# Optimization experiments

Hardware: AMD Instinct MI355X
Metric: run time of the kernel (lower is better)

The kernel has to match this reference:

```python
import jax, jax.numpy as jnp
import numpy as np

N_NODES = 100000
N_EDGES = 1600000
HIDDEN = 64
N_LAYERS = 3
N_CLASSES = 2
N_GRAPHS = 128
NEG_SLOPE = 0.2  # PyG GATConv default negative_slope


def setup_inputs() -> dict:
    key = jax.random.key(0)
    ks = jax.random.split(key, 8)
    x = jax.random.randint(ks[0], (N_NODES,), 0, 2)
    edge_index = jax.random.randint(ks[1], (2, N_EDGES), 0, N_NODES)
    batch = jnp.sort(jax.random.randint(ks[2], (N_NODES,), 0, N_GRAPHS))
    scale = 1.0 / np.sqrt(HIDDEN)
    embed_table = jax.random.normal(ks[3], (2, HIDDEN), jnp.float32)
    Ws = jax.random.normal(ks[4], (N_LAYERS, HIDDEN, HIDDEN), jnp.float32) * scale
    a_srcs = jax.random.normal(ks[5], (N_LAYERS, HIDDEN), jnp.float32) * scale
    a_dsts = jax.random.normal(ks[6], (N_LAYERS, HIDDEN), jnp.float32) * scale
    biases = jnp.zeros((N_LAYERS, HIDDEN), jnp.float32)
    W_out = jax.random.normal(ks[7], (HIDDEN, N_CLASSES), jnp.float32) * scale
    b_out = jnp.zeros((N_CLASSES,), jnp.float32)
    return {"x": x, "edge_index": edge_index, "batch": batch,
            "embed_table": embed_table, "Ws": Ws, "a_srcs": a_srcs,
            "a_dsts": a_dsts, "biases": biases, "W_out": W_out, "b_out": b_out}


def _gat_layer(h, src, dst, W, a_s, a_d, b):
    # h: [N, D]; src/dst: [E'] (self loops included) -> PyG GATConv, heads=1
    hW = h @ W                                   # [N, D]
    e = jax.nn.leaky_relu((hW @ a_s)[src] + (hW @ a_d)[dst], NEG_SLOPE)  # [E']
    m = jax.ops.segment_max(e, dst, num_segments=N_NODES)               # stable softmax per dst
    ex = jnp.exp(e - m[dst])
    denom = jax.ops.segment_sum(ex, dst, num_segments=N_NODES)
    alpha = ex / denom[dst]                      # [E']
    out = jax.ops.segment_sum(hW[src] * alpha[:, None], dst, num_segments=N_NODES)
    return out + b


def reference(x, edge_index, batch, embed_table, Ws, a_srcs, a_dsts, biases, W_out, b_out):
    loop = jnp.arange(N_NODES)
    src = jnp.concatenate([edge_index[0], loop])  # PyG add_self_loops=True
    dst = jnp.concatenate([edge_index[1], loop])
    h = embed_table[x]                            # [N, D]
    for l in range(N_LAYERS):
        h = _gat_layer(h, src, dst, Ws[l], a_srcs[l], a_dsts[l], biases[l])
        if l < N_LAYERS - 1:
            h = jax.nn.relu(h)
    sums = jax.ops.segment_sum(h, batch, num_segments=N_GRAPHS)
    counts = jax.ops.segment_sum(jnp.ones((N_NODES,), h.dtype), batch, num_segments=N_GRAPHS)
    pooled = sums / jnp.maximum(counts, 1.0)[:, None]  # global_mean_pool
    return pooled @ W_out + b_out                      # [G, num_classes]
```

## Files before the change

### kernel.cpp

```cpp
#include <hip/hip_runtime.h>
#include <hip/hip_bf16.h>
#include <float.h>

#define N_NODES 100000
#define N_EDGES 1600000
#define HIDDEN 64
#define N_GRAPHS 128
#define NEG_SLOPE 0.2f
#define ETOT (N_EDGES + N_NODES)

#define BSHIFT 9
#define NB ((N_NODES + 511) >> BSHIFT)
#define PAIR_CHUNK 4096
#define PAIR_BLOCKS ((N_EDGES + PAIR_CHUNK - 1) / PAIR_CHUNK)
#define XBIT_BLOCKS ((N_NODES + 255) / 256)
#define TBL_BLOCKS (NLVL / 8)
#define CAP 12288

#define NREP 64
#define REP_STRIDE 272
#define NLVL 512

__device__ __forceinline__ int sb0(unsigned u) { return (int)((unsigned)(u << 24)) >> 24; }
__device__ __forceinline__ int sb1(unsigned u) { return (int)((unsigned)(u << 16)) >> 24; }
__device__ __forceinline__ int sb2(unsigned u) { return (int)((unsigned)(u << 8)) >> 24; }
__device__ __forceinline__ int sb3(unsigned u) { return (int)u >> 24; }


__global__ __launch_bounds__(256) void k_prep(
    const int* __restrict__ x,
    int* __restrict__ gcnt, float* __restrict__ pool_acc,
    unsigned* __restrict__ xb)
{
    int t = threadIdx.x, b = blockIdx.x;
    if (b == 0 && t < NB) gcnt[t] = 0;
    if (b < NREP && t < 2 * N_GRAPHS) pool_acc[b * REP_STRIDE + t] = 0.f;
    int i = b * 256 + t;
    int lane = t & 63;
    bool bb = (i < N_NODES) && (x[i] != 0);
    unsigned long long m = __ballot(bb);
    int wid = i >> 6;
    if (i < N_NODES + 64) {
        if (lane == 0) xb[wid * 2] = (unsigned)m;
        if (lane == 32) xb[wid * 2 + 1] = (unsigned)(m >> 32);
    }
}


__global__ __launch_bounds__(512) void k_scatter(
    const int* __restrict__ e0, const int* __restrict__ e1,
    const unsigned* __restrict__ xb, int* __restrict__ gcnt,
    int* __restrict__ pairs,
    const float* __restrict__ embed, const float* __restrict__ Ws,
    const float* __restrict__ biases, const float* __restrict__ a_srcs,
    const float* __restrict__ a_dsts, const float* __restrict__ W_out,
    unsigned char* __restrict__ Tq8, float* __restrict__ Tscl,
    float* __restrict__ Ts1s, float* __restrict__ Ts1d,
    float* __restrict__ sparams, float* __restrict__ Vp)
{
    __shared__ int hcnt[NB];
    __shared__ int base[NB];
    __shared__ int lstart[NB];
    __shared__ int tot[256];
    __shared__ int staged[PAIR_CHUNK];
    __shared__ int sdest[PAIR_CHUNK];
    int t = threadIdx.x, b = blockIdx.x;

    if (b >= PAIR_BLOCKS + TBL_BLOCKS) {
        int w = t >> 6, f = t & 63;
        if (w < 4) {
            const float* W3 = Ws + 8192;
            float s = 0.f;
#pragma unroll 8
            for (int m = 0; m < 64; ++m) {
                float u = (w == 0) ? a_srcs[128 + m]
                        : (w == 1) ? W_out[2 * m]
                        : (w == 2) ? W_out[2 * m + 1]
                        : a_dsts[128 + m];
                s = fmaf(W3[f * 64 + m], u, s);
            }
            Vp[f * 4 + w] = s;
        }
        return;
    }

    if (b >= PAIR_BLOCKS) {
        int l = (b - PAIR_BLOCKS) * 8 + (t >> 6);
        int f = t & 63;
        float r0 = 0.f, r1 = 0.f;
#pragma unroll 8
        for (int k = 0; k < 64; ++k) {
            float w = Ws[k * 64 + f];
            r0 = fmaf(embed[k], w, r0);
            r1 = fmaf(embed[64 + k], w, r1);
        }
        if (l == 0) {
            float as = a_srcs[f], ad = a_dsts[f];
            float t0 = r0 * as, t1 = r1 * as, t2 = r0 * ad, t3 = r1 * ad;
#pragma unroll
            for (int off = 32; off >= 1; off >>= 1) {
                t0 += __shfl_xor(t0, off); t1 += __shfl_xor(t1, off);
                t2 += __shfl_xor(t2, off); t3 += __shfl_xor(t3, off);
            }
            if (f == 0) { sparams[0] = t0; sparams[1] = t1; sparams[2] = t2; sparams[3] = t3; }
        }
        if (l == 1) {
            float b2 = biases[128 + f];
            float t4 = b2 * W_out[f * 2];
            float t5 = b2 * W_out[f * 2 + 1];
#pragma unroll
            for (int off = 32; off >= 1; off >>= 1) {
                t4 += __shfl_xor(t4, off); t5 += __shfl_xor(t5, off);
            }
            if (f == 0) { sparams[4] = t4; sparams[5] = t5; }
        }
        float c1 = (float)l * (1.f / (NLVL - 1));
        float o = fmaxf(biases[f] + r0 + c1 * (r1 - r0), 0.f);
        const float* W1 = Ws + 4096;
        float h = 0.f;
#pragma unroll 8
        for (int k = 0; k < 64; ++k) h = fmaf(__shfl(o, k), W1[k * 64 + f], h);
        float ss = h * a_srcs[64 + f];
        float sd = h * a_dsts[64 + f];
        float am = fabsf(h);
#pragma unroll
        for (int off = 32; off >= 1; off >>= 1) {
            ss += __shfl_xor(ss, off);
            sd += __shfl_xor(sd, off);
            am = fmaxf(am, __shfl_xor(am, off));
        }
        float iscl = (am > 0.f) ? 127.f / am : 0.f;
        Tq8[l * 64 + f] = (unsigned char)(__float2int_rn(h * iscl) & 255);
        if (f == 0) { Tscl[l] = am * (1.f / 127.f); Ts1s[l] = ss; Ts1d[l] = sd; }
        return;
    }

    if (t < NB) hcnt[t] = 0;
    __syncthreads();
    int ebase = b * PAIR_CHUNK;
    int ecount = min(PAIR_CHUNK, N_EDGES - ebase);
    for (int i = 4 * t; i < ecount; i += 2048) {
        int4 d4 = *(const int4*)(e1 + ebase + i);
        atomicAdd(&hcnt[d4.x >> BSHIFT], 1);
        atomicAdd(&hcnt[d4.y >> BSHIFT], 1);
        atomicAdd(&hcnt[d4.z >> BSHIFT], 1);
        atomicAdd(&hcnt[d4.w >> BSHIFT], 1);
    }
    __syncthreads();
    int v = (t < NB) ? hcnt[t] : 0;
    if (t < 256) tot[t] = v;
    __syncthreads();
    for (int off = 1; off < 256; off <<= 1) {
        int u = (t >= off && t < 256) ? tot[t - off] : 0;
        __syncthreads();
        if (t < 256) tot[t] += u;
        __syncthreads();
    }
    if (t < NB) {
        lstart[t] = tot[t] - v;
        base[t] = v ? atomicAdd(&gcnt[t], v) : 0;
        hcnt[t] = 0;
    }
    __syncthreads();
    for (int i = 4 * t; i < ecount; i += 2048) {
        int4 s4 = *(const int4*)(e0 + ebase + i);
        int4 d4 = *(const int4*)(e1 + ebase + i);
        int ss[4] = {s4.x, s4.y, s4.z, s4.w};
        int dd[4] = {d4.x, d4.y, d4.z, d4.w};
#pragma unroll
        for (int j = 0; j < 4; ++j) {
            int s = ss[j], d = dd[j];
            int xv = (xb[s >> 5] >> (s & 31)) & 1;
            int B = d >> BSHIFT;
            int idx = atomicAdd(&hcnt[B], 1);
            int lp = lstart[B] + idx;
            staged[lp] = (xv << 26) | ((d & 511) << 17) | s;
            sdest[lp] = B * CAP + base[B] + idx;
        }
    }
    __syncthreads();
    for (int i = t; i < ecount; i += 512)
        pairs[sdest[i]] = staged[i];
}

__global__ __launch_bounds__(1024) void k_csr_bucket(
    const int* __restrict__ pairs, const int* __restrict__ gcnt,
    const int* __restrict__ x, const float* __restrict__ sparams,
    int* __restrict__ rowptr, int* __restrict__ col,
    unsigned short* __restrict__ cidx)
{
    __shared__ int deg[512];
    __shared__ int excl[512];
    __shared__ int cnt2[512];
    __shared__ int wsum[16];
    __shared__ int p0sh;
    int b = blockIdx.x;
    int t = threadIdx.x;
    int nb = b << BSHIFT;
    int nodes = min(512, N_NODES - nb);

    int pv = (t < b) ? gcnt[t] : 0;
#pragma unroll
    for (int off = 32; off >= 1; off >>= 1) pv += __shfl_xor(pv, off);
    if ((t & 63) == 0) wsum[t >> 6] = pv;
    __syncthreads();
    if (t == 0) {
        int s = 0;
#pragma unroll
        for (int i = 0; i < 16; ++i) s += wsum[i];
        p0sh = s;
    }

    int xself = 0;
    if (t < 512) {
        xself = (t < nodes) ? (x[nb + t] & 1) : 0;
        deg[t] = (t < nodes) ? (1 | (xself << 16)) : 0;
        cnt2[t] = 1;
    }
    __syncthreads();
    int cnt = gcnt[b];
    int pbase = b * CAP;
    int cnt4 = cnt & ~3;
    for (int i = 4 * t; i < cnt4; i += 4096) {
        int4 p4 = *(const int4*)(pairs + pbase + i);
        atomicAdd(&deg[(p4.x >> 17) & 511], 1 | (((p4.x >> 26) & 1) << 16));
        atomicAdd(&deg[(p4.y >> 17) & 511], 1 | (((p4.y >> 26) & 1) << 16));
        atomicAdd(&deg[(p4.z >> 17) & 511], 1 | (((p4.z >> 26) & 1) << 16));
        atomicAdd(&deg[(p4.w >> 17) & 511], 1 | (((p4.w >> 26) & 1) << 16));
    }
    for (int i = cnt4 + t; i < cnt; i += 1024) {
        int p = pairs[pbase + i];
        atomicAdd(&deg[(p >> 17) & 511], 1 | (((p >> 26) & 1) << 16));
    }
    __syncthreads();

    int packed = (t < 512) ? deg[t] : 0;
    int val = packed & 0xFFFF;
    int kx = packed >> 16;
    if (t < nodes) {
        float ss0 = sparams[0], ss1 = sparams[1];
        float sd = xself ? sparams[3] : sparams[2];
        float e0 = ss0 + sd; e0 = (e0 >= 0.f) ? e0 : NEG_SLOPE * e0;
        float e1 = ss1 + sd; e1 = (e1 >= 0.f) ? e1 : NEG_SLOPE * e1;
        float pp0 = __expf(e0), pp1 = __expf(e1);
        float kn = (float)kx, dn = (float)(val - kx);
        float c1 = kn * pp1 / (dn * pp0 + kn * pp1);
        cidx[nb + t] = (unsigned short)__float2int_rn(c1 * (float)(NLVL - 1));
    }

    int xx = val;
#pragma unroll
    for (int off = 1; off < 64; off <<= 1) {
        int y = __shfl_up(xx, off);
        if ((t & 63) >= off) xx += y;
    }
    if ((t & 63) == 63 && t < 512) wsum[t >> 6] = xx;
    __syncthreads();
    if (t == 0) {
        int s = 0;
#pragma unroll
        for (int i = 0; i < 8; ++i) { int v = wsum[i]; wsum[i] = s; s += v; }
    }
    __syncthreads();
    int ex = xx - val + wsum[t >> 6];
    if (t < 512) excl[t] = ex;

    int p0 = p0sh;
    int colbase = p0 + nb;
    if (t < nodes) {
        rowptr[nb + t] = colbase + ex;
        col[colbase + ex] = nb + t;
    }
    if (b == NB - 1 && t == 0) rowptr[N_NODES] = ETOT;
    __syncthreads();
    for (int i = 4 * t; i < cnt4; i += 4096) {
        int4 p4 = *(const int4*)(pairs + pbase + i);
        int pp[4] = {p4.x, p4.y, p4.z, p4.w};
#pragma unroll
        for (int j = 0; j < 4; ++j) {
            int li = (pp[j] >> 17) & 511;
            int pos = colbase + excl[li] + atomicAdd(&cnt2[li], 1);
            col[pos] = pp[j] & 0x1FFFF;
        }
    }
    for (int i = cnt4 + t; i < cnt; i += 1024) {
        int p = pairs[pbase + i];
        int li = (p >> 17) & 511;
        int pos = colbase + excl[li] + atomicAdd(&cnt2[li], 1);
        col[pos] = p & 0x1FFFF;
    }
}


__global__ __launch_bounds__(256) void k_agg1(
    const unsigned char* __restrict__ Tq8, const float* __restrict__ Tscl,
    const float* __restrict__ Ts1s, const float* __restrict__ Ts1d,
    const unsigned short* __restrict__ cidx, const int* __restrict__ col,
    const int* __restrict__ rowptr, const float* __restrict__ bias,
    const float4* __restrict__ Vp, float4* __restrict__ szz)
{
    __shared__ float2 stash[4][64];
    int t = threadIdx.x;
    int wave = t >> 6, lane = t & 63;
    int h = lane >> 5, hl = lane & 31;
    int base = blockIdx.x * 8 + wave * 2;
    if (base >= N_NODES) return;
    const char* hb = (const char*)Tq8;

    int node = base + h;
    bool valid = (node < N_NODES);
    int row = 0, end = 0;
    if (valid) { row = rowptr[node]; end = rowptr[node + 1]; }
    int deg = end - row;
    int degO = __shfl_xor(deg, 32);
    bool fast = (deg <= 32) && (degO <= 32);

    if (fast) {
        int idx = 0;
        float p = 0.f, sc = 0.f;
        if (hl < deg) idx = cidx[col[row + hl]];
        float sdi = Ts1d[__shfl(idx, h * 32)];
        if (hl < deg) {
            float ee = Ts1s[idx] + sdi;
            ee = (ee >= 0.f) ? ee : NEG_SLOPE * ee;
            p = __expf(ee);
            sc = Tscl[idx];
        }
        stash[wave][lane] = make_float2(p * sc, __int_as_float(idx * 64));

        int q = hl >> 4;
        int f = hl & 15;
        int f4 = f * 4;
        int sb = h * 32;
        float a0 = 0.f, a1 = 0.f, a2 = 0.f, a3 = 0.f;
        int degr = (deg + 7) & ~7;
        for (int j = q; j < degr; j += 8) {
            float2 e0 = stash[wave][sb + j];
            float2 e1 = stash[wave][sb + j + 2];
            float2 e2 = stash[wave][sb + j + 4];
            float2 e3 = stash[wave][sb + j + 6];
            unsigned v0 = *(const unsigned*)(hb + (__float_as_int(e0.y) + f4));
            unsigned v1 = *(const unsigned*)(hb + (__float_as_int(e1.y) + f4));
            unsigned v2 = *(const unsigned*)(hb + (__float_as_int(e2.y) + f4));
            unsigned v3 = *(const unsigned*)(hb + (__float_as_int(e3.y) + f4));
            a0 = fmaf(e0.x, (float)sb0(v0), a0);
            a1 = fmaf(e0.x, (float)sb1(v0), a1);
            a2 = fmaf(e0.x, (float)sb2(v0), a2);
            a3 = fmaf(e0.x, (float)sb3(v0), a3);
            a0 = fmaf(e1.x, (float)sb0(v1), a0);
            a1 = fmaf(e1.x, (float)sb1(v1), a1);
            a2 = fmaf(e1.x, (float)sb2(v1), a2);
            a3 = fmaf(e1.x, (float)sb3(v1), a3);
            a0 = fmaf(e2.x, (float)sb0(v2), a0);
            a1 = fmaf(e2.x, (float)sb1(v2), a1);
            a2 = fmaf(e2.x, (float)sb2(v2), a2);
            a3 = fmaf(e2.x, (float)sb3(v2), a3);
            a0 = fmaf(e3.x, (float)sb0(v3), a0);
            a1 = fmaf(e3.x, (float)sb1(v3), a1);
            a2 = fmaf(e3.x, (float)sb2(v3), a2);
            a3 = fmaf(e3.x, (float)sb3(v3), a3);
        }
        float denom = p;
#pragma unroll
        for (int off = 16; off >= 1; off >>= 1) denom += __shfl_xor(denom, off);
        float inv = 1.f / denom;
        a0 += __shfl_xor(a0, 16);
        a1 += __shfl_xor(a1, 16);
        a2 += __shfl_xor(a2, 16);
        a3 += __shfl_xor(a3, 16);

        float4 pr = make_float4(0.f, 0.f, 0.f, 0.f);
        if (hl < 16 && valid) {
            float4 bb = *(const float4*)&bias[4 * f];
            float h0 = fmaxf(fmaf(a0, inv, bb.x), 0.f);
            float h1 = fmaxf(fmaf(a1, inv, bb.y), 0.f);
            float h2 = fmaxf(fmaf(a2, inv, bb.z), 0.f);
            float h3 = fmaxf(fmaf(a3, inv, bb.w), 0.f);
            float4 w0 = Vp[4 * f + 0];
            float4 w1 = Vp[4 * f + 1];
            float4 w2 = Vp[4 * f + 2];
            float4 w3 = Vp[4 * f + 3];
            pr.x = h0 * w0.x + h1 * w1.x + h2 * w2.x + h3 * w3.x;
            pr.y = h0 * w0.y + h1 * w1.y + h2 * w2.y + h3 * w3.y;
            pr.z = h0 * w0.z + h1 * w1.z + h2 * w2.z + h3 * w3.z;
            pr.w = h0 * w0.w + h1 * w1.w + h2 * w2.w + h3 * w3.w;
        }
#pragma unroll
        for (int off = 8; off >= 1; off >>= 1) {
            pr.x += __shfl_xor(pr.x, off);
            pr.y += __shfl_xor(pr.y, off);
            pr.z += __shfl_xor(pr.z, off);
            pr.w += __shfl_xor(pr.w, off);
        }
        if (hl == 0 && valid) szz[node] = pr;
    } else {
        for (int s = 0; s < 2; ++s) {
            int nd = base + s;
            if (nd >= N_NODES) continue;
            int r = rowptr[nd], e = rowptr[nd + 1];
            float sdi = Ts1d[cidx[nd]];
            float m = -FLT_MAX;
            for (int j = r + lane; j < e; j += 64) {
                float ee = Ts1s[cidx[col[j]]] + sdi;
                ee = (ee >= 0.f) ? ee : NEG_SLOPE * ee;
                m = fmaxf(m, ee);
            }
#pragma unroll
            for (int off = 32; off >= 1; off >>= 1) m = fmaxf(m, __shfl_xor(m, off));
            float denom = 0.f;
            for (int j = r + lane; j < e; j += 64) {
                float ee = Ts1s[cidx[col[j]]] + sdi;
                ee = (ee >= 0.f) ? ee : NEG_SLOPE * ee;
                denom += __expf(ee - m);
            }
#pragma unroll
            for (int off = 32; off >= 1; off >>= 1) denom += __shfl_xor(denom, off);
            float inv = 1.f / denom;
            float acc = 0.f;
            for (int j = r; j < e; ++j) {
                int idxj = cidx[col[j]];
                float ee = Ts1s[idxj] + sdi;
                ee = (ee >= 0.f) ? ee : NEG_SLOPE * ee;
                float w = __expf(ee - m) * inv * Tscl[idxj];
                int bq = (int)(signed char)Tq8[idxj * 64 + lane];
                acc = fmaf(w, (float)bq, acc);
            }
            float hv = fmaxf(acc + bias[lane], 0.f);
            float4 vp = Vp[lane];
            float4 pr = make_float4(hv * vp.x, hv * vp.y, hv * vp.z, hv * vp.w);
#pragma unroll
            for (int off = 32; off >= 1; off >>= 1) {
                pr.x += __shfl_xor(pr.x, off);
                pr.y += __shfl_xor(pr.y, off);
                pr.z += __shfl_xor(pr.z, off);
                pr.w += __shfl_xor(pr.w, off);
            }
            if (lane == 0) szz[nd] = pr;
        }
    }
}


__global__ __launch_bounds__(256) void k_pool2(
    const float4* __restrict__ szz, const int* __restrict__ col,
    const int* __restrict__ rowptr, const int* __restrict__ batch,
    float* __restrict__ pool_acc)
{
    __shared__ int rp2[33];
    int t = threadIdx.x;
    int wave = t >> 6, lane = t & 63;
    int h = lane >> 5, hl = lane & 31;
    int nb0 = blockIdx.x * 32;
    if (t < 33) {
        int n = nb0 + t;
        rp2[t] = (n <= N_NODES) ? rowptr[n] : ETOT;
    }
    __syncthreads();
    float* rep = pool_acc + ((blockIdx.x * 4 + wave) & (NREP - 1)) * REP_STRIDE;

    int gcur = -1;
    float acc0 = 0.f, acc1 = 0.f;

#pragma unroll
    for (int i = 0; i < 4; ++i) {
        int nls = wave * 8 + 2 * i + h;
        int node = nb0 + nls;
        bool valid = (node < N_NODES);
        int row = valid ? rp2[nls] : 0;
        int end = valid ? rp2[nls + 1] : 0;
        int deg = end - row;
        int degO = __shfl_xor(deg, 32);
        bool fast = (deg <= 32) && (degO <= 32);
        float r0 = 0.f, r1 = 0.f;

        if (fast) {
            float sdi = valid ? szz[node].w : 0.f;
            float p = 0.f, zy = 0.f, zz = 0.f;
            if (hl < deg) {
                int c = col[row + hl];
                float4 sz = szz[c];
                float ee = sz.x + sdi;
                ee = (ee >= 0.f) ? ee : NEG_SLOPE * ee;
                p = __expf(ee);
                zy = sz.y; zz = sz.z;
            }
            float n0 = p * zy, n1 = p * zz, dn = p;
#pragma unroll
            for (int off = 16; off >= 1; off >>= 1) {
                n0 += __shfl_xor(n0, off);
                n1 += __shfl_xor(n1, off);
                dn += __shfl_xor(dn, off);
            }
            float inv = 1.f / dn;
            r0 = n0 * inv; r1 = n1 * inv;
        } else {
            float rr0[2], rr1[2];
#pragma unroll
            for (int s = 0; s < 2; ++s) {
                rr0[s] = rr1[s] = 0.f;
                int nds = wave * 8 + 2 * i + s;
                int nd = nb0 + nds;
                if (nd >= N_NODES) continue;
                int r = rp2[nds], e = rp2[nds + 1];
                float sdi = szz[nd].w;
                float n0 = 0.f, n1 = 0.f, dn = 0.f;
                for (int j = r + lane; j < e; j += 64) {
                    int c = col[j];
                    float4 sz = szz[c];
                    float ee = sz.x + sdi;
                    ee = (ee >= 0.f) ? ee : NEG_SLOPE * ee;
                    float p = __expf(ee);
                    n0 = fmaf(p, sz.y, n0);
                    n1 = fmaf(p, sz.z, n1);
                    dn += p;
                }
#pragma unroll
                for (int off = 32; off >= 1; off >>= 1) {
                    n0 += __shfl_xor(n0, off);
                    n1 += __shfl_xor(n1, off);
                    dn += __shfl_xor(dn, off);
                }
                float inv = 1.f / dn;
                rr0[s] = n0 * inv; rr1[s] = n1 * inv;
            }
            r0 = rr0[h]; r1 = rr1[h];
        }

        if (hl == 0 && valid) {
            int g = batch[node];
            if (g != gcur) {
                if (gcur >= 0) {
                    atomicAdd(&rep[gcur * 2], acc0);
                    atomicAdd(&rep[gcur * 2 + 1], acc1);
                }
                gcur = g; acc0 = r0; acc1 = r1;
            } else {
                acc0 += r0; acc1 += r1;
            }
        }
    }
    if (hl == 0 && gcur >= 0) {
        atomicAdd(&rep[gcur * 2], acc0);
        atomicAdd(&rep[gcur * 2 + 1], acc1);
    }
}


__device__ __forceinline__ int lower_bound_dev(const int* __restrict__ a, int n, int v) {
    int lo = 0, hi = n;
    while (lo < hi) {
        int mid = (lo + hi) >> 1;
        if (a[mid] < v) lo = mid + 1; else hi = mid;
    }
    return lo;
}

__global__ void k_head(const float* __restrict__ pool_acc,
                       const int* __restrict__ batch,
                       const float* __restrict__ b_out,
                       const float* __restrict__ sparams,
                       float* __restrict__ out)
{
    int t = threadIdx.x;
    if (t < 2 * N_GRAPHS) {
        float s = 0.f;
#pragma unroll 8
        for (int r = 0; r < NREP; ++r) s += pool_acc[r * REP_STRIDE + t];
        int g = t >> 1, c = t & 1;
        int start = lower_bound_dev(batch, N_NODES, g);
        int end = lower_bound_dev(batch, N_NODES, g + 1);
        float cnt = fmaxf((float)(end - start), 1.f);
        out[t] = s / cnt + sparams[4 + c] + b_out[c];
    }
}


extern "C" void kernel_launch(void* const* d_in, const int* in_sizes, int n_in,
                              void* d_out, int out_size, void* d_ws, size_t ws_size,
                              hipStream_t stream) {
    const int*   x       = (const int*)d_in[0];
    const int*   edge    = (const int*)d_in[1];
    const int*   batch   = (const int*)d_in[2];
    const float* embed   = (const float*)d_in[3];
    const float* Ws      = (const float*)d_in[4];
    const float* a_srcs  = (const float*)d_in[5];
    const float* a_dsts  = (const float*)d_in[6];
    const float* biases  = (const float*)d_in[7];
    const float* W_out   = (const float*)d_in[8];
    const float* b_out   = (const float*)d_in[9];
    float* out = (float*)d_out;

    char* ws = (char*)d_ws;
    size_t off = 0;
    auto alloc = [&](size_t bytes) -> void* {
        void* p = ws + off;
        off += (bytes + 255) & ~(size_t)255;
        return p;
    };
    float4* szz     = (float4*)alloc((size_t)N_NODES * sizeof(float4));
    unsigned short* cidx = (unsigned short*)alloc((size_t)N_NODES * sizeof(unsigned short));
    int*   rowptr   = (int*)alloc((size_t)(N_NODES + 1) * sizeof(int));
    int*   colA     = (int*)alloc((size_t)ETOT * sizeof(int));
    int*   gcnt     = (int*)alloc((size_t)NB * sizeof(int));
    float* pool_acc = (float*)alloc((size_t)(NREP * REP_STRIDE) * sizeof(float));
    unsigned* xb    = (unsigned*)alloc((size_t)3232 * sizeof(unsigned));
    unsigned char* Tq8 = (unsigned char*)alloc((size_t)NLVL * 64);
    float* Tscl     = (float*)alloc((size_t)NLVL * sizeof(float));
    float* Ts1s     = (float*)alloc((size_t)NLVL * sizeof(float));
    float* Ts1d     = (float*)alloc((size_t)NLVL * sizeof(float));
    float* sparams  = (float*)alloc((size_t)8 * sizeof(float));
    float* Vp       = (float*)alloc((size_t)256 * sizeof(float));
    int*   pairs    = (int*)alloc((size_t)NB * CAP * sizeof(int));

    const int* e0 = edge;
    const int* e1 = edge + N_EDGES;

    k_prep<<<XBIT_BLOCKS, 256, 0, stream>>>(x, gcnt, pool_acc, xb);
    k_scatter<<<PAIR_BLOCKS + TBL_BLOCKS + 1, 512, 0, stream>>>(
        e0, e1, xb, gcnt, pairs,
        embed, Ws, biases, a_srcs, a_dsts, W_out,
        Tq8, Tscl, Ts1s, Ts1d, sparams, Vp);
    k_csr_bucket<<<NB, 1024, 0, stream>>>(pairs, gcnt, x, sparams, rowptr, colA, cidx);

    k_agg1<<<(N_NODES + 7) / 8, 256, 0, stream>>>(
        Tq8, Tscl, Ts1s, Ts1d, cidx, colA, rowptr, biases + 64,
        (const float4*)Vp, szz);
    k_pool2<<<(N_NODES + 31) / 32, 256, 0, stream>>>(
        szz, colA, rowptr, batch, pool_acc);
    k_head<<<1, 256, 0, stream>>>(pool_acc, batch, b_out, sparams, out);
}
```

Baseline: 181.9 us.

## Stage quantized lookup tables in LDS and make agg kernel grid-stride persistent

The aggregation kernel now copies the 512-level int8 feature table, its attention and scale tables, the projection vector and the bias into shared memory once per block. Each block then loops over node groups with a grid stride over 2048 blocks of 512 threads. This moves the random per-edge table gathers from global/L2 into LDS and spreads the cost of the table load over many nodes. In exchange each block uses about 40KB of LDS, which can reduce occupancy, and every block pays an upfront copy before any work starts.

```diff
diff --git a/kernel.cpp b/kernel.cpp
--- a/kernel.cpp
+++ b/kernel.cpp
@@ -20,6 +20,8 @@
 #define NREP 64
 #define REP_STRIDE 272
 #define NLVL 512
+#define AGG_GROUPS ((N_NODES + 15) / 16)
+#define AGG_BLOCKS 2048
 
 __device__ __forceinline__ int sb0(unsigned u) { return (int)((unsigned)(u << 24)) >> 24; }
 __device__ __forceinline__ int sb1(unsigned u) { return (int)((unsigned)(u << 16)) >> 24; }
@@ -292,150 +294,163 @@
 }
 
 
-__global__ __launch_bounds__(256) void k_agg1(
+__global__ __launch_bounds__(512) void k_agg1(
     const unsigned char* __restrict__ Tq8, const float* __restrict__ Tscl,
     const float* __restrict__ Ts1s, const float* __restrict__ Ts1d,
     const unsigned short* __restrict__ cidx, const int* __restrict__ col,
     const int* __restrict__ rowptr, const float* __restrict__ bias,
     const float4* __restrict__ Vp, float4* __restrict__ szz)
 {
-    __shared__ float2 stash[4][64];
+    __shared__ unsigned char TqL[NLVL * 64];
+    __shared__ float S1s[NLVL], S1d[NLVL], Scl[NLVL];
+    __shared__ float4 VpL[64];
+    __shared__ float4 biasL[16];
+    __shared__ float2 stash[8][64];
     int t = threadIdx.x;
+
+    for (int i = t; i < NLVL * 16; i += 512)
+        ((int*)TqL)[i] = ((const int*)Tq8)[i];
+    if (t < NLVL) { S1s[t] = Ts1s[t]; S1d[t] = Ts1d[t]; Scl[t] = Tscl[t]; }
+    if (t < 64) VpL[t] = Vp[t];
+    if (t < 16) biasL[t] = *(const float4*)&bias[4 * t];
+    __syncthreads();
+
     int wave = t >> 6, lane = t & 63;
     int h = lane >> 5, hl = lane & 31;
-    int base = blockIdx.x * 8 + wave * 2;
-    if (base >= N_NODES) return;
-    const char* hb = (const char*)Tq8;
-
-    int node = base + h;
-    bool valid = (node < N_NODES);
-    int row = 0, end = 0;
-    if (valid) { row = rowptr[node]; end = rowptr[node + 1]; }
-    int deg = end - row;
-    int degO = __shfl_xor(deg, 32);
-    bool fast = (deg <= 32) && (degO <= 32);
-
-    if (fast) {
-        int idx = 0;
-        float p = 0.f, sc = 0.f;
-        if (hl < deg) idx = cidx[col[row + hl]];
-        float sdi = Ts1d[__shfl(idx, h * 32)];
-        if (hl < deg) {
-            float ee = Ts1s[idx] + sdi;
-            ee = (ee >= 0.f) ? ee : NEG_SLOPE * ee;
-            p = __expf(ee);
-            sc = Tscl[idx];
-        }
-        stash[wave][lane] = make_float2(p * sc, __int_as_float(idx * 64));
-
-        int q = hl >> 4;
-        int f = hl & 15;
-        int f4 = f * 4;
-        int sb = h * 32;
-        float a0 = 0.f, a1 = 0.f, a2 = 0.f, a3 = 0.f;
-        int degr = (deg + 7) & ~7;
-        for (int j = q; j < degr; j += 8) {
-            float2 e0 = stash[wave][sb + j];
-            float2 e1 = stash[wave][sb + j + 2];
-            float2 e2 = stash[wave][sb + j + 4];
-            float2 e3 = stash[wave][sb + j + 6];
-            unsigned v0 = *(const unsigned*)(hb + (__float_as_int(e0.y) + f4));
-            unsigned v1 = *(const unsigned*)(hb + (__float_as_int(e1.y) + f4));
-            unsigned v2 = *(const unsigned*)(hb + (__float_as_int(e2.y) + f4));
-            unsigned v3 = *(const unsigned*)(hb + (__float_as_int(e3.y) + f4));
-            a0 = fmaf(e0.x, (float)sb0(v0), a0);
-            a1 = fmaf(e0.x, (float)sb1(v0), a1);
-            a2 = fmaf(e0.x, (float)sb2(v0), a2);
-            a3 = fmaf(e0.x, (float)sb3(v0), a3);
-            a0 = fmaf(e1.x, (float)sb0(v1), a0);
-            a1 = fmaf(e1.x, (float)sb1(v1), a1);
-            a2 = fmaf(e1.x, (float)sb2(v1), a2);
-            a3 = fmaf(e1.x, (float)sb3(v1), a3);
-            a0 = fmaf(e2.x, (float)sb0(v2), a0);
-            a1 = fmaf(e2.x, (float)sb1(v2), a1);
-            a2 = fmaf(e2.x, (float)sb2(v2), a2);
-            a3 = fmaf(e2.x, (float)sb3(v2), a3);
-            a0 = fmaf(e3.x, (float)sb0(v3), a0);
-            a1 = fmaf(e3.x, (float)sb1(v3), a1);
-            a2 = fmaf(e3.x, (float)sb2(v3), a2);
-            a3 = fmaf(e3.x, (float)sb3(v3), a3);
-        }
-        float denom = p;
-#pragma unroll
-        for (int off = 16; off >= 1; off >>= 1) denom += __shfl_xor(denom, off);
-        float inv = 1.f / denom;
-        a0 += __shfl_xor(a0, 16);
-        a1 += __shfl_xor(a1, 16);
-        a2 += __shfl_xor(a2, 16);
-        a3 += __shfl_xor(a3, 16);
-
-        float4 pr = make_float4(0.f, 0.f, 0.f, 0.f);
-        if (hl < 16 && valid) {
-            float4 bb = *(const float4*)&bias[4 * f];
-            float h0 = fmaxf(fmaf(a0, inv, bb.x), 0.f);
-            float h1 = fmaxf(fmaf(a1, inv, bb.y), 0.f);
-            float h2 = fmaxf(fmaf(a2, inv, bb.z), 0.f);
-            float h3 = fmaxf(fmaf(a3, inv, bb.w), 0.f);
-            float4 w0 = Vp[4 * f + 0];
-            float4 w1 = Vp[4 * f + 1];
-            float4 w2 = Vp[4 * f + 2];
-            float4 w3 = Vp[4 * f + 3];
-            pr.x = h0 * w0.x + h1 * w1.x + h2 * w2.x + h3 * w3.x;
-            pr.y = h0 * w0.y + h1 * w1.y + h2 * w2.y + h3 * w3.y;
-            pr.z = h0 * w0.z + h1 * w1.z + h2 * w2.z + h3 * w3.z;
-            pr.w = h0 * w0.w + h1 * w1.w + h2 * w2.w + h3 * w3.w;
-        }
-#pragma unroll
-        for (int off = 8; off >= 1; off >>= 1) {
-            pr.x += __shfl_xor(pr.x, off);
-            pr.y += __shfl_xor(pr.y, off);
-            pr.z += __shfl_xor(pr.z, off);
-            pr.w += __shfl_xor(pr.w, off);
-        }
-        if (hl == 0 && valid) szz[node] = pr;
-    } else {
-        for (int s = 0; s < 2; ++s) {
-            int nd = base + s;
-            if (nd >= N_NODES) continue;
-            int r = rowptr[nd], e = rowptr[nd + 1];
-            float sdi = Ts1d[cidx[nd]];
-            float m = -FLT_MAX;
-            for (int j = r + lane; j < e; j += 64) {
-                float ee = Ts1s[cidx[col[j]]] + sdi;
+    const char* hb = (const char*)TqL;
+
+    for (int grp = blockIdx.x; grp < AGG_GROUPS; grp += gridDim.x) {
+        int base = grp * 16 + wave * 2;
+        int node = base + h;
+        bool valid = (node < N_NODES);
+        int row = 0, end = 0;
+        if (valid) { row = rowptr[node]; end = rowptr[node + 1]; }
+        int deg = end - row;
+        int degO = __shfl_xor(deg, 32);
+        bool fast = (deg <= 32) && (degO <= 32);
+
+        if (fast) {
+            int idx = 0;
+            float p = 0.f, sc = 0.f;
+            if (hl < deg) idx = cidx[col[row + hl]];
+            float sdi = S1d[__shfl(idx, h * 32)];
+            if (hl < deg) {
+                float ee = S1s[idx] + sdi;
                 ee = (ee >= 0.f) ? ee : NEG_SLOPE * ee;
-                m = fmaxf(m, ee);
-            }
-#pragma unroll
-            for (int off = 32; off >= 1; off >>= 1) m = fmaxf(m, __shfl_xor(m, off));
-            float denom = 0.f;
-            for (int j = r + lane; j < e; j += 64) {
-                float ee = Ts1s[cidx[col[j]]] + sdi;
-                ee = (ee >= 0.f) ? ee : NEG_SLOPE * ee;
-                denom += __expf(ee - m);
-            }
-#pragma unroll
-            for (int off = 32; off >= 1; off >>= 1) denom += __shfl_xor(denom, off);
+                p = __expf(ee);
+                sc = Scl[idx];
+            }
+            stash[wave][lane] = make_float2(p * sc, __int_as_float(idx * 64));
+
+            int q = hl >> 4;
+            int f = hl & 15;
+            int f4 = f * 4;
+            int sb = h * 32;
+            float a0 = 0.f, a1 = 0.f, a2 = 0.f, a3 = 0.f;
+            int degr = (deg + 7) & ~7;
+            for (int j = q; j < degr; j += 8) {
+                float2 e0 = stash[wave][sb + j];
+                float2 e1 = stash[wave][sb + j + 2];
+                float2 e2 = stash[wave][sb + j + 4];
+                float2 e3 = stash[wave][sb + j + 6];
+                unsigned v0 = *(const unsigned*)(hb + (__float_as_int(e0.y) + f4));
+                unsigned v1 = *(const unsigned*)(hb + (__float_as_int(e1.y) + f4));
+                unsigned v2 = *(const unsigned*)(hb + (__float_as_int(e2.y) + f4));
+                unsigned v3 = *(const unsigned*)(hb + (__float_as_int(e3.y) + f4));
+                a0 = fmaf(e0.x, (float)sb0(v0), a0);
+                a1 = fmaf(e0.x, (float)sb1(v0), a1);
+                a2 = fmaf(e0.x, (float)sb2(v0), a2);
+                a3 = fmaf(e0.x, (float)sb3(v0), a3);
+                a0 = fmaf(e1.x, (float)sb0(v1), a0);
+                a1 = fmaf(e1.x, (float)sb1(v1), a1);
+                a2 = fmaf(e1.x, (float)sb2(v1), a2);
+                a3 = fmaf(e1.x, (float)sb3(v1), a3);
+                a0 = fmaf(e2.x, (float)sb0(v2), a0);
+                a1 = fmaf(e2.x, (float)sb1(v2), a1);
+                a2 = fmaf(e2.x, (float)sb2(v2), a2);
+                a3 = fmaf(e2.x, (float)sb3(v2), a3);
+                a0 = fmaf(e3.x, (float)sb0(v3), a0);
+                a1 = fmaf(e3.x, (float)sb1(v3), a1);
+                a2 = fmaf(e3.x, (float)sb2(v3), a2);
+                a3 = fmaf(e3.x, (float)sb3(v3), a3);
+            }
+            float denom = p;
+#pragma unroll
+            for (int off = 16; off >= 1; off >>= 1) denom += __shfl_xor(denom, off);
             float inv = 1.f / denom;
-            float acc = 0.f;
-            for (int j = r; j < e; ++j) {
-                int idxj = cidx[col[j]];
-                float ee = Ts1s[idxj] + sdi;
-                ee = (ee >= 0.f) ? ee : NEG_SLOPE * ee;
-                float w = __expf(ee - m) * inv * Tscl[idxj];
-                int bq = (int)(signed char)Tq8[idxj * 64 + lane];
-                acc = fmaf(w, (float)bq, acc);
-            }
-            float hv = fmaxf(acc + bias[lane], 0.f);
-            float4 vp = Vp[lane];
-            float4 pr = make_float4(hv * vp.x, hv * vp.y, hv * vp.z, hv * vp.w);
-#pragma unroll
-            for (int off = 32; off >= 1; off >>= 1) {
+            a0 += __shfl_xor(a0, 16);
+            a1 += __shfl_xor(a1, 16);
+            a2 += __shfl_xor(a2, 16);
+            a3 += __shfl_xor(a3, 16);
+
+            float4 pr = make_float4(0.f, 0.f, 0.f, 0.f);
+            if (hl < 16 && valid) {
+                float4 bb = biasL[f];
+                float h0 = fmaxf(fmaf(a0, inv, bb.x), 0.f);
+                float h1 = fmaxf(fmaf(a1, inv, bb.y), 0.f);
+                float h2 = fmaxf(fmaf(a2, inv, bb.z), 0.f);
+                float h3 = fmaxf(fmaf(a3, inv, bb.w), 0.f);
+                float4 w0 = VpL[4 * f + 0];
+                float4 w1 = VpL[4 * f + 1];
+                float4 w2 = VpL[4 * f + 2];
+                float4 w3 = VpL[4 * f + 3];
+                pr.x = h0 * w0.x + h1 * w1.x + h2 * w2.x + h3 * w3.x;
+                pr.y = h0 * w0.y + h1 * w1.y + h2 * w2.y + h3 * w3.y;
+                pr.z = h0 * w0.z + h1 * w1.z + h2 * w2.z + h3 * w3.z;
+                pr.w = h0 * w0.w + h1 * w1.w + h2 * w2.w + h3 * w3.w;
+            }
+#pragma unroll
+            for (int off = 8; off >= 1; off >>= 1) {
                 pr.x += __shfl_xor(pr.x, off);
                 pr.y += __shfl_xor(pr.y, off);
                 pr.z += __shfl_xor(pr.z, off);
                 pr.w += __shfl_xor(pr.w, off);
             }
-            if (lane == 0) szz[nd] = pr;
+            if (hl == 0 && valid) szz[node] = pr;
+        } else {
+            for (int s = 0; s < 2; ++s) {
+                int nd = base + s;
+                if (nd >= N_NODES) continue;
+                int r = rowptr[nd], e = rowptr[nd + 1];
+                float sdi = S1d[cidx[nd]];
+                float m = -FLT_MAX;
+                for (int j = r + lane; j < e; j += 64) {
+                    float ee = S1s[cidx[col[j]]] + sdi;
+                    ee = (ee >= 0.f) ? ee : NEG_SLOPE * ee;
+                    m = fmaxf(m, ee);
+                }
+#pragma unroll
+                for (int off = 32; off >= 1; off >>= 1) m = fmaxf(m, __shfl_xor(m, off));
+                float denom = 0.f;
+                for (int j = r + lane; j < e; j += 64) {
+                    float ee = S1s[cidx[col[j]]] + sdi;
+                    ee = (ee >= 0.f) ? ee : NEG_SLOPE * ee;
+                    denom += __expf(ee - m);
+                }
+#pragma unroll
+                for (int off = 32; off >= 1; off >>= 1) denom += __shfl_xor(denom, off);
+                float inv = 1.f / denom;
+                float acc = 0.f;
+                for (int j = r; j < e; ++j) {
+                    int idxj = cidx[col[j]];
+                    float ee = S1s[idxj] + sdi;
+                    ee = (ee >= 0.f) ? ee : NEG_SLOPE * ee;
+                    float w = __expf(ee - m) * inv * Scl[idxj];
+                    int bq = (int)(signed char)TqL[idxj * 64 + lane];
+                    acc = fmaf(w, (float)bq, acc);
+                }
+                float hv = fmaxf(acc + bias[lane], 0.f);
+                float4 vp = VpL[lane];
+                float4 pr = make_float4(hv * vp.x, hv * vp.y, hv * vp.z, hv * vp.w);
+#pragma unroll
+                for (int off = 32; off >= 1; off >>= 1) {
+                    pr.x += __shfl_xor(pr.x, off);
+                    pr.y += __shfl_xor(pr.y, off);
+                    pr.z += __shfl_xor(pr.z, off);
+                    pr.w += __shfl_xor(pr.w, off);
+                }
+                if (lane == 0) szz[nd] = pr;
+            }
         }
     }
 }
@@ -622,7 +637,7 @@
         Tq8, Tscl, Ts1s, Ts1d, sparams, Vp);
     k_csr_bucket<<<NB, 1024, 0, stream>>>(pairs, gcnt, x, sparams, rowptr, colA, cidx);
 
-    k_agg1<<<(N_NODES + 7) / 8, 256, 0, stream>>>(
+    k_agg1<<<AGG_BLOCKS, 512, 0, stream>>>(
         Tq8, Tscl, Ts1s, Ts1d, cidx, colA, rowptr, biases + 64,
         (const float4*)Vp, szz);
     k_pool2<<<(N_NODES + 31) / 32, 256, 0, stream>>>(
```

Result: no change. 183.4 us (+0.8%).
